# Kernel tuning notes

Hardware: AMD Instinct MI355X
Metric: run time of the kernel (lower is better)

## Reference

```python
import jax, jax.numpy as jnp
import numpy as np
from jax import lax

EPS_NORM = 1e-12   # F.normalize default eps
KS = 3             # fixed 3x3 window
K2 = KS * KS
MIN_CONN, MAX_CONN = 1, 8
NUM_GROUPS = 16    # largest divisor <=16 of C=128
GN_EPS = 1e-5


def _unfold3x3_reflect(x):
    # x: [B,C,H,W] -> patches [B,C,9,H,W] (reflect-padded 3x3 neighborhoods)
    B, C, H, W = x.shape
    p = jnp.pad(x, ((0, 0), (0, 0), (1, 1), (1, 1)), mode='reflect')
    pats = [p[:, :, dy:dy + H, dx:dx + W] for dy in range(KS) for dx in range(KS)]
    return jnp.stack(pats, axis=2)


def _df_counts(x):
    # DFDetector: mean over C, fixed Laplacian conv (zero pad), abs, per-batch min-max norm
    B = x.shape[0]
    avg = jnp.mean(x, axis=1, keepdims=True)  # [B,1,H,W]
    kern = jnp.array([[0., -1., 0.], [-1., 4., -1.], [0., -1., 0.]],
                     dtype=x.dtype).reshape(1, 1, 3, 3)
    df = jnp.abs(lax.conv_general_dilated(
        avg, kern, window_strides=(1, 1), padding=((1, 1), (1, 1)),
        dimension_numbers=('NCHW', 'OIHW', 'NCHW')))
    dmin = df.reshape(B, -1).min(axis=1).reshape(B, 1, 1, 1)
    dmax = df.reshape(B, -1).max(axis=1).reshape(B, 1, 1, 1)
    dn = (df - dmin) / (dmax - dmin + 1e-8)
    return MIN_CONN + jnp.round(dn * (MAX_CONN - MIN_CONN))  # [B,1,H,W], values in [1,8]


def _group_norm(x, w, b):
    B, C, H, W = x.shape
    g = x.reshape(B, NUM_GROUPS, -1)
    mu = g.mean(-1, keepdims=True)
    var = g.var(-1, keepdims=True)  # biased, matches torch GroupNorm
    g = (g - mu) * lax.rsqrt(var + GN_EPS)
    return g.reshape(B, C, H, W) * w[None, :, None, None] + b[None, :, None, None]


def setup_inputs() -> dict:
    key = jax.random.key(0)
    ks = jax.random.split(key, 7)
    B, C, H, W = 8, 128, 96, 96
    return {
        'x': jax.random.normal(ks[0], (B, C, H, W), jnp.float32),
        'gn_weight': jax.random.uniform(ks[1], (C,), jnp.float32, 0.5, 1.5),
        'gn_bias': jax.random.normal(ks[2], (C,), jnp.float32) * 0.1,
        'w1': jax.random.normal(ks[3], (2 * C, C), jnp.float32) * 0.02,
        'b1': jax.random.normal(ks[4], (2 * C,), jnp.float32) * 0.02,
        'w2': jax.random.normal(ks[5], (C, 2 * C), jnp.float32) * 0.02,
        'b2': jax.random.normal(ks[6], (C,), jnp.float32) * 0.02,
    }


def reference(x, gn_weight, gn_bias, w1, b1, w2, b2):
    B, C, H, W = x.shape
    P = H * W
    # per-pixel connection counts (integer k in [1,8]); non-differentiable in original
    counts = lax.stop_gradient(_df_counts(x))
    kvals = jnp.minimum(counts, K2).astype(jnp.int32).reshape(B, 1, P)

    patches = _unfold3x3_reflect(x).reshape(B, C, K2, P)
    xc = x.reshape(B, C, P)
    # L2 normalize over channel dim (F.normalize, eps=1e-12)
    cn = xc / jnp.maximum(jnp.linalg.norm(xc, axis=1, keepdims=True), EPS_NORM)
    pn = patches / jnp.maximum(jnp.linalg.norm(patches, axis=1, keepdims=True), EPS_NORM)

    sim = jnp.einsum('bcp,bckp->bkp', cn, pn)          # [B,9,P] cosine sims
    order = jnp.argsort(-sim, axis=1)                   # descending (== topk order)
    top_sim = jnp.take_along_axis(sim, order, axis=1)
    mask = jnp.arange(K2)[None, :, None] < kvals        # rank < k -> selected
    wts = jnp.exp(top_sim) * mask
    wts = wts / jnp.sum(wts, axis=1, keepdims=True)     # softmax over selected sims

    pat_sorted = jnp.take_along_axis(patches, order[:, None, :, :], axis=2)
    out = jnp.einsum('bckp,bkp->bcp', pat_sorted, wts).reshape(B, C, H, W)

    enhanced = out + _group_norm(x, gn_weight, gn_bias)
    h = jax.nn.relu(jnp.einsum('oi,bihw->bohw', w1, enhanced) + b1[None, :, None, None])
    ffn = jnp.einsum('oi,bihw->bohw', w2, h) + b2[None, :, None, None]
    return enhanced + ffn
```

## Files before the change

kernel.cpp:

```cpp
#include <hip/hip_runtime.h>

#define BD 8
#define CD 128
#define HD 96
#define WD 96
#define PD 9216
#define ND 73728

typedef __attribute__((ext_vector_type(8))) short short8;
typedef __attribute__((ext_vector_type(4))) float f32x4;

__device__ inline float bfu2f(unsigned int u) { return __uint_as_float(u << 16); }
__device__ inline unsigned short f2bfu(float f) {
  unsigned int u = __float_as_uint(f);
  u += 0x7fffu + ((u >> 16) & 1u);
  return (unsigned short)(u >> 16);
}

template<bool F32>
__device__ __forceinline__ float ldv(const void* __restrict__ p, size_t i) {
  if constexpr (F32) return ((const float*)p)[i];
  else return bfu2f(((const unsigned short*)p)[i]);
}

__global__ void k_detect(const unsigned int* __restrict__ xw, int* __restrict__ dcnt) {
  __shared__ int wl[4], we[4];
  const int t = threadIdx.x;
  uint4 w = ((const uint4*)xw)[blockIdx.x * 256 + t];
  int lz = (int)((w.x & 0xFFFFu) == 0u) + (int)((w.y & 0xFFFFu) == 0u) +
           (int)((w.z & 0xFFFFu) == 0u) + (int)((w.w & 0xFFFFu) == 0u);
  int e2 = (int)(((w.x >> 7) & 0xFFu) == 0xFFu) + (int)(((w.y >> 7) & 0xFFu) == 0xFFu) +
           (int)(((w.z >> 7) & 0xFFu) == 0xFFu) + (int)(((w.w >> 7) & 0xFFu) == 0xFFu);
  #pragma unroll
  for (int off = 32; off; off >>= 1) {
    lz += __shfl_down(lz, off);
    e2 += __shfl_down(e2, off);
  }
  if ((t & 63) == 0) { wl[t >> 6] = lz; we[t >> 6] = e2; }
  __syncthreads();
  if (t == 0) {
    dcnt[blockIdx.x] = wl[0] + wl[1] + wl[2] + wl[3];
    dcnt[64 + blockIdx.x] = we[0] + we[1] + we[2] + we[3];
  }
}

__global__ void k_cvt(const void* __restrict__ w1, const void* __restrict__ w2,
                      const void* __restrict__ gw, const void* __restrict__ gb,
                      const void* __restrict__ b1, const void* __restrict__ b2,
                      const int* __restrict__ dcnt,
                      unsigned short* __restrict__ wc, float* __restrict__ prm,
                      int* __restrict__ flag, unsigned long long* __restrict__ dmm) {
  __shared__ int sflag;
  const int t = threadIdx.x;
  if (t < 64) {
    int lz = dcnt[t], e2 = dcnt[64 + t];
    #pragma unroll
    for (int off = 32; off; off >>= 1) {
      lz += __shfl_down(lz, off);
      e2 += __shfl_down(e2, off);
    }
    if (t == 0) sflag = (lz > 4096 || e2 > 0) ? 1 : 0;
  }
  __syncthreads();
  const bool f32 = sflag != 0;
  const int blk = blockIdx.x;
  if (blk < 256) {
    int i = blk * 256 + t;
    if (i < 32768)
      wc[i] = f32 ? f2bfu(((const float*)w1)[i]) : ((const unsigned short*)w1)[i];
    else {
      int u = i - 32768;
      wc[i] = f32 ? f2bfu(((const float*)w2)[u]) : ((const unsigned short*)w2)[u];
    }
  } else {
    for (int i = t; i < 640; i += 256) {
      float v;
      if (i < 128)      v = f32 ? ((const float*)gw)[i]       : bfu2f(((const unsigned short*)gw)[i]);
      else if (i < 256) v = f32 ? ((const float*)gb)[i - 128] : bfu2f(((const unsigned short*)gb)[i - 128]);
      else if (i < 512) v = f32 ? ((const float*)b1)[i - 256] : bfu2f(((const unsigned short*)b1)[i - 256]);
      else              v = f32 ? ((const float*)b2)[i - 512] : bfu2f(((const unsigned short*)b2)[i - 512]);
      prm[i] = v;
    }
    if (t < 8) dmm[t] = 0x7FEFFFFFFFFFFFFFULL;
    else if (t < 16) dmm[t - 8 + 8] = 0ULL;
    if (t == 16) *flag = sflag;
  }
}

template<bool F32>
__device__ __forceinline__ void stats_body(const void* __restrict__ x,
                                           double* __restrict__ avg, double* __restrict__ nrm,
                                           double* __restrict__ nrm2, double* __restrict__ gpart,
                                           int lb) {
  const int t = threadIdx.x;
  const int gp0 = lb * 256;
  const int b = gp0 / PD, p0 = gp0 - b * PD;
  const size_t base = (size_t)b * CD * PD + p0 + t;
  double s = 0.0, q = 0.0;
  double qq0 = 0.0, qq1 = 0.0, qq2 = 0.0, qq3 = 0.0;
  double* gslot = gpart + (size_t)(lb * 4 + (t >> 6)) * 32;
  #pragma unroll
  for (int g = 0; g < 16; ++g) {
    double gs = 0.0, gq = 0.0;
    #pragma unroll
    for (int j = 0; j < 8; ++j) {
      const int c = g * 8 + j;
      double dv = (double)ldv<F32>(x, base + (size_t)c * PD);
      s += dv;
      q += dv * dv;
      if (g < 4) qq0 += dv * dv;
      else if (g < 8) qq1 += dv * dv;
      else if (g < 12) qq2 += dv * dv;
      else qq3 += dv * dv;
      gs += dv;
      gq += dv * dv;
    }
    #pragma unroll
    for (int off = 32; off; off >>= 1) {
      gs += __shfl_down(gs, off);
      gq += __shfl_down(gq, off);
    }
    if ((t & 63) == 0) { gslot[g * 2] = gs; gslot[g * 2 + 1] = gq; }
  }
  avg[gp0 + t] = s * (1.0 / 128.0);
  nrm[gp0 + t] = sqrt(q);
  nrm2[gp0 + t] = ((qq0 + qq1) + qq2) + qq3;
}
__global__ __launch_bounds__(256) void k_stats(const void* __restrict__ x,
                                               const int* __restrict__ flag,
                                               double* __restrict__ avg,
                                               double* __restrict__ nrm,
                                               double* __restrict__ nrm2,
                                               double* __restrict__ gpart) {
  const int lb = (blockIdx.x & 7) * 36 + (blockIdx.x >> 3);
  if (*flag) stats_body<true>(x, avg, nrm, nrm2, gpart, lb);
  else stats_body<false>(x, avg, nrm, nrm2, gpart, lb);
}

__device__ inline double lap_df(const double* __restrict__ a, int b, int y, int x) {
  const double* ab = a + (size_t)b * PD;
  double v = 4.0 * ab[y * WD + x];
  if (y > 0)      v -= ab[(y - 1) * WD + x];
  if (y < HD - 1) v -= ab[(y + 1) * WD + x];
  if (x > 0)      v -= ab[y * WD + x - 1];
  if (x < WD - 1) v -= ab[y * WD + x + 1];
  return fabs(v);
}

__global__ void k_mg(const double* __restrict__ avg, unsigned long long* __restrict__ dmm,
                     double* __restrict__ dfb, const double* __restrict__ gpart,
                     float* __restrict__ gn) {
  __shared__ double red[8];
  const int t = threadIdx.x;
  if (blockIdx.x < 288) {
    const int lb = ((int)blockIdx.x & 7) * 36 + ((int)blockIdx.x >> 3);
    int gp = lb * 256 + t;
    int b = gp / PD, p = gp - b * PD;
    double df = lap_df(avg, b, p / WD, p % WD);
    dfb[gp] = df;
    double mn = df, mx = df;
    #pragma unroll
    for (int off = 32; off; off >>= 1) {
      mn = fmin(mn, __shfl_down(mn, off));
      mx = fmax(mx, __shfl_down(mx, off));
    }
    if ((t & 63) == 0) { red[t >> 6] = mn; red[4 + (t >> 6)] = mx; }
    __syncthreads();
    if (t == 0) {
      mn = fmin(fmin(red[0], red[1]), fmin(red[2], red[3]));
      mx = fmax(fmax(red[4], red[5]), fmax(red[6], red[7]));
      atomicMin(&dmm[b], (unsigned long long)__double_as_longlong(mn));
      atomicMax(&dmm[b + 8], (unsigned long long)__double_as_longlong(mx));
    }
  } else {
    const int bg = blockIdx.x - 288;
    const int b = bg >> 4, g = bg & 15;
    double s = 0.0, q = 0.0;
    if (t < 144) {
      const double* pp = gpart + (size_t)(b * 144 + t) * 32 + g * 2;
      s = pp[0];
      q = pp[1];
    }
    #pragma unroll
    for (int off = 32; off; off >>= 1) {
      s += __shfl_down(s, off);
      q += __shfl_down(q, off);
    }
    if ((t & 63) == 0) { red[t >> 6] = s; red[4 + (t >> 6)] = q; }
    __syncthreads();
    if (t == 0) {
      double S = ((red[0] + red[1]) + red[2]) + red[3];
      double Q = ((red[4] + red[5]) + red[6]) + red[7];
      double mu = S / 73728.0;
      double var = Q / 73728.0 - mu * mu;
      gn[bg] = (float)mu;
      gn[128 + bg] = (float)(1.0 / sqrt(var + 1e-5));
    }
  }
}

template<bool F32>
__device__ __forceinline__ void ipg_body(const void* __restrict__ x,
                                         const double* __restrict__ nrm,
                                         const double* __restrict__ nrm2,
                                         const double* __restrict__ dfb,
                                         const unsigned long long* __restrict__ dmm,
                                         const float* __restrict__ gn,
                                         const float* __restrict__ prm,
                                         unsigned short* __restrict__ eg,
                                         float* __restrict__ tileF,
                                         double* __restrict__ nsl, double* __restrict__ nsl2) {
  float4* tile4 = (float4*)tileF;
  const float* gwf = prm;
  const float* gbf = prm + 128;

  const int t = threadIdx.x;
  const int lb = (blockIdx.x & 7) * 144 + (blockIdx.x >> 3);
  const int b = lb / 144;
  const int tid = lb - b * 144;
  const int ty = tid / 12, tx = tid - ty * 12;
  const int y0 = ty * 8, x0 = tx * 8;

  {
    const int hp = t & 127;
    if (hp < 100) {
      int hr = hp / 10, hc = hp - hr * 10;
      int gy = y0 - 1 + hr; gy = gy < 0 ? -gy : (gy >= HD ? 2 * HD - 2 - gy : gy);
      int gx = x0 - 1 + hc; gx = gx < 0 ? -gx : (gx >= WD ? 2 * WD - 2 - gx : gx);
      const size_t pbase = (size_t)b * CD * PD + (size_t)gy * WD + gx;
      const int sw = hp & 7;
      #pragma unroll
      for (int it = 0; it < 16; ++it) {
        int s = it * 2 + (t >> 7);
        size_t cb = pbase + (size_t)(4 * s) * PD;
        float4 v;
        v.x = ldv<F32>(x, cb);
        v.y = ldv<F32>(x, cb + PD);
        v.z = ldv<F32>(x, cb + 2 * PD);
        v.w = ldv<F32>(x, cb + 3 * PD);
        tile4[(hp * 32 + s) ^ sw] = v;
      }
      if (t < 100) nsl[t] = nrm[b * PD + gy * WD + gx];
    }
    if (t >= 128 && t < 192) {
      int a2 = t - 128;
      nsl2[a2] = nrm2[b * PD + (y0 + (a2 >> 3)) * WD + x0 + (a2 & 7)];
    }
  }
  __syncthreads();

  const int a = t >> 2, q = t & 3;
  const int yl = a >> 3, xl = a & 7;
  const int y = y0 + yl, xx = x0 + xl;
  const int p = y * WD + xx;
  const int cpix = (yl + 1) * 10 + (xl + 1);
  const int cub = cpix * 32 + q * 8, csw = cpix & 7;

  double sd[9];
  {
    float cv[32];
    #pragma unroll
    for (int j4 = 0; j4 < 8; ++j4)
      *(float4*)(cv + 4 * j4) = tile4[(cub + j4) ^ csw];
    #pragma unroll
    for (int k = 0; k < 9; ++k) {
      if (k == 4) continue;
      int dy = k / 3, dx = k - dy * 3;
      int pix = (yl + dy) * 10 + (xl + dx);
      int ub = pix * 32 + q * 8, sw = pix & 7;
      double acc = 0.0;
      #pragma unroll
      for (int seg = 0; seg < 8; ++seg) {
        float4 nv = tile4[(ub + seg) ^ sw];
        acc += (double)cv[seg * 4 + 0] * (double)nv.x;
        acc += (double)cv[seg * 4 + 1] * (double)nv.y;
        acc += (double)cv[seg * 4 + 2] * (double)nv.z;
        acc += (double)cv[seg * 4 + 3] * (double)nv.w;
      }
      double v1 = __shfl_down(acc, 1);
      double v2 = __shfl_down(acc, 2);
      double v3 = __shfl_down(acc, 3);
      sd[k] = ((acc + v1) + v2) + v3;
    }
  }

  float wv[9];
  #pragma unroll
  for (int j = 0; j < 9; ++j) wv[j] = 0.f;
  if (q == 0) {
    double dmin = __longlong_as_double((long long)dmm[b]);
    double dmax = __longlong_as_double((long long)dmm[b + 8]);
    double df = dfb[b * PD + p];
    double dn = (df - dmin) / (dmax - dmin + 1e-8);
    int kk = 1 + (int)rint(dn * 7.0);
    kk = kk < 1 ? 1 : (kk > 8 ? 8 : kk);

    sd[4] = nsl2[a];
    double np_ = fmax(nsl[cpix], 1e-12);
    #pragma unroll
    for (int k = 0; k < 9; ++k) {
      int dy = k / 3, dx = k - dy * 3;
      double nq = fmax(nsl[(yl + dy) * 10 + (xl + dx)], 1e-12);
      sd[k] = sd[k] / (np_ * nq);
    }
    float w[9];
    float wsum = 0.f;
    #pragma unroll
    for (int j = 0; j < 9; ++j) {
      int rank = 0;
      #pragma unroll
      for (int i = 0; i < 9; ++i)
        rank += (sd[i] > sd[j]) || (sd[i] == sd[j] && i < j);
      w[j] = (rank < kk) ? expf((float)sd[j]) : 0.f;
      wsum += w[j];
    }
    float inv = 1.f / wsum;
    #pragma unroll
    for (int j = 0; j < 9; ++j) wv[j] = w[j] * inv;
  }
  #pragma unroll
  for (int j = 0; j < 9; ++j) wv[j] = __shfl(wv[j], (t & 63) & ~3);

  {
    float og[32];
    #pragma unroll
    for (int j = 0; j < 32; ++j) og[j] = 0.f;
    #pragma unroll
    for (int k = 0; k < 9; ++k) {
      int dy = k / 3, dx = k - dy * 3;
      int pix = (yl + dy) * 10 + (xl + dx);
      int ub = pix * 32 + q * 8, sw = pix & 7;
      #pragma unroll
      for (int seg = 0; seg < 8; ++seg) {
        float4 nv = tile4[(ub + seg) ^ sw];
        og[seg * 4 + 0] += wv[k] * nv.x;
        og[seg * 4 + 1] += wv[k] * nv.y;
        og[seg * 4 + 2] += wv[k] * nv.z;
        og[seg * 4 + 3] += wv[k] * nv.w;
      }
    }
    const int g16 = b * 16;
    unsigned short* egr = eg + (size_t)(b * PD + p) * 128 + q * 32;
    #pragma unroll
    for (int seg = 0; seg < 4; ++seg) {
      float4 cA = tile4[(cub + seg * 2) ^ csw];
      float4 cB = tile4[(cub + seg * 2 + 1) ^ csw];
      float cvv[8] = {cA.x, cA.y, cA.z, cA.w, cB.x, cB.y, cB.z, cB.w};
      int g = q * 4 + seg;
      float mu = gn[g16 + g], rs = gn[128 + g16 + g];
      unsigned int pkd[4];
      #pragma unroll
      for (int j = 0; j < 8; ++j) {
        int c = q * 32 + seg * 8 + j;
        float e = og[seg * 8 + j] + (cvv[j] - mu) * rs * gwf[c] + gbf[c];
        unsigned int h = (unsigned int)f2bfu(e);
        if (j & 1) pkd[j >> 1] |= h << 16;
        else pkd[j >> 1] = h;
      }
      uint4 v; v.x = pkd[0]; v.y = pkd[1]; v.z = pkd[2]; v.w = pkd[3];
      *(uint4*)(egr + seg * 8) = v;
    }
  }
}
__global__ __launch_bounds__(256, 3) void k_ipg(const void* __restrict__ x,
                                                const int* __restrict__ flag,
                                                const double* __restrict__ nrm,
                                                const double* __restrict__ nrm2,
                                                const double* __restrict__ dfb,
                                                const unsigned long long* __restrict__ dmm,
                                                const float* __restrict__ gn,
                                                const float* __restrict__ prm,
                                                unsigned short* __restrict__ eg) {
  __shared__ float tileF[12800];
  __shared__ double nsl[100];
  __shared__ double nsl2[64];
  if (*flag) ipg_body<true>(x, nrm, nrm2, dfb, dmm, gn, prm, eg, tileF, nsl, nsl2);
  else ipg_body<false>(x, nrm, nrm2, dfb, dmm, gn, prm, eg, tileF, nsl, nsl2);
}

__global__ __launch_bounds__(256, 3) void k_ffn(const unsigned short* __restrict__ eg,
                                                const float* __restrict__ prm,
                                                const unsigned short* __restrict__ wc,
                                                float* __restrict__ outp) {
  __shared__ unsigned short et[64][136];
  __shared__ unsigned short Hl[64][264];
  const float* b1f = prm + 256;
  const float* b2f = prm + 512;

  const int t = threadIdx.x;
  const int lb = (blockIdx.x & 7) * 144 + (blockIdx.x >> 3);
  const int gp0 = lb * 64;
  const int b = gp0 / PD, p0b = gp0 - b * PD;

  const unsigned short* wc1 = wc;
  const unsigned short* wc2 = wc + 32768;
  const int lane = t & 63, wave = t >> 6;
  const int r16 = lane & 15, quad = lane >> 4;

  {
    const uint4* eg4 = (const uint4*)(eg + (size_t)gp0 * 128);
    #pragma unroll
    for (int it = 0; it < 4; ++it) {
      int lin = it * 256 + t;
      int row = lin >> 4, c8 = lin & 15;
      *(uint4*)&et[row][c8 * 8] = eg4[lin];
    }
  }
  short8 wb1[16];
  #pragma unroll
  for (int kk = 0; kk < 4; ++kk)
    #pragma unroll
    for (int nt = 0; nt < 4; ++nt)
      wb1[kk * 4 + nt] = *(const short8*)(wc1 + (size_t)(wave * 64 + nt * 16 + r16) * 128 + kk * 32 + quad * 8);
  __syncthreads();

  f32x4 acc[16];
  #pragma unroll
  for (int i = 0; i < 16; ++i) acc[i] = (f32x4){0.f, 0.f, 0.f, 0.f};
  #pragma unroll
  for (int kk = 0; kk < 4; ++kk) {
    short8 afm[4];
    #pragma unroll
    for (int m = 0; m < 4; ++m)
      afm[m] = *(const short8*)&et[m * 16 + r16][kk * 32 + quad * 8];
    #pragma unroll
    for (int nt = 0; nt < 4; ++nt)
      #pragma unroll
      for (int m = 0; m < 4; ++m)
        acc[m * 4 + nt] = __builtin_amdgcn_mfma_f32_16x16x32_bf16(afm[m], wb1[kk * 4 + nt], acc[m * 4 + nt], 0, 0, 0);
  }
  #pragma unroll
  for (int nt = 0; nt < 4; ++nt) {
    int n = wave * 64 + nt * 16 + r16;
    float bias = b1f[n];
    #pragma unroll
    for (int m = 0; m < 4; ++m)
      #pragma unroll
      for (int r = 0; r < 4; ++r)
        Hl[m * 16 + quad * 4 + r][n] = f2bfu(fmaxf(acc[m * 4 + nt][r] + bias, 0.f));
  }
  short8 wb2[16];
  #pragma unroll
  for (int kk = 0; kk < 8; ++kk)
    #pragma unroll
    for (int nt = 0; nt < 2; ++nt)
      wb2[kk * 2 + nt] = *(const short8*)(wc2 + (size_t)(wave * 32 + nt * 16 + r16) * 256 + kk * 32 + quad * 8);
  __syncthreads();

  f32x4 acc2[8];
  #pragma unroll
  for (int i = 0; i < 8; ++i) acc2[i] = (f32x4){0.f, 0.f, 0.f, 0.f};
  #pragma unroll
  for (int kk = 0; kk < 8; ++kk) {
    short8 afm[4];
    #pragma unroll
    for (int m = 0; m < 4; ++m)
      afm[m] = *(const short8*)&Hl[m * 16 + r16][kk * 32 + quad * 8];
    #pragma unroll
    for (int nt = 0; nt < 2; ++nt)
      #pragma unroll
      for (int m = 0; m < 4; ++m)
        acc2[m * 2 + nt] = __builtin_amdgcn_mfma_f32_16x16x32_bf16(afm[m], wb2[kk * 2 + nt], acc2[m * 2 + nt], 0, 0, 0);
  }
  #pragma unroll
  for (int nt = 0; nt < 2; ++nt) {
    int n = wave * 32 + nt * 16 + r16;
    float bias = b2f[n];
    #pragma unroll
    for (int m = 0; m < 4; ++m) {
      int mloc0 = m * 16 + quad * 4;
      float4 o;
      o.x = acc2[m * 2 + nt][0] + bias + bfu2f(et[mloc0 + 0][n]);
      o.y = acc2[m * 2 + nt][1] + bias + bfu2f(et[mloc0 + 1][n]);
      o.z = acc2[m * 2 + nt][2] + bias + bfu2f(et[mloc0 + 2][n]);
      o.w = acc2[m * 2 + nt][3] + bias + bfu2f(et[mloc0 + 3][n]);
      *(float4*)(outp + (size_t)(b * CD + n) * PD + p0b + mloc0) = o;
    }
  }
}

extern "C" void kernel_launch(void* const* d_in, const int* in_sizes, int n_in,
                              void* d_out, int out_size, void* d_ws, size_t ws_size,
                              hipStream_t stream) {
  const void* x  = d_in[0];
  const void* gw = d_in[1];
  const void* gb = d_in[2];
  const void* w1 = d_in[3];
  const void* b1 = d_in[4];
  const void* w2 = d_in[5];
  const void* b2 = d_in[6];
  float* out = (float*)d_out;

  char* ws = (char*)d_ws;
  int* flag = (int*)ws;
  int* dcnt = (int*)(ws + 16);
  unsigned long long* dmm = (unsigned long long*)(ws + 640);
  float* gn = (float*)(ws + 768);
  float* prm = (float*)(ws + 1792);
  unsigned short* wc = (unsigned short*)(ws + 4352);
  double* avg = (double*)(ws + 135424);
  double* nrm = (double*)(ws + 725248);
  double* nrm2 = (double*)(ws + 1315072);
  double* gpart = (double*)(ws + 1904896);
  double* dfb = (double*)(ws + 2199808);
  unsigned short* eg = (unsigned short*)(ws + 2789632);

  k_detect<<<64, 256, 0, stream>>>((const unsigned int*)x, dcnt);
  k_cvt<<<257, 256, 0, stream>>>(w1, w2, gw, gb, b1, b2, dcnt, wc, prm, flag, dmm);
  k_stats<<<288, 256, 0, stream>>>(x, flag, avg, nrm, nrm2, gpart);
  k_mg<<<416, 256, 0, stream>>>(avg, dmm, dfb, gpart, gn);
  k_ipg<<<ND / 64, 256, 0, stream>>>(x, flag, nrm, nrm2, dfb, dmm, gn, prm, eg);
  k_ffn<<<ND / 64, 256, 0, stream>>>(eg, prm, wc, out);
}
```

Before: 210.6 us.

## Transpose input to pixel-major layout in stats pass for coalesced halo loads

Replaces the stats kernel with one that loads 64-pixel by 128-channel tiles, computes the same statistics, and writes a pixel-major (channel-contiguous) copy of x to workspace. The patch kernel then gathers its 10x10 halo with contiguous float4 or ushort4 loads per pixel instead of strided per-channel scalar loads. This removes uncoalesced, channel-strided reads in k_ipg. In exchange it adds a full extra write and read of x through the workspace, and the bf16 path rounds the copy. The per-pixel stats now come from a single thread per pixel looping over shared memory.

```diff
diff --git a/kernel.cpp b/kernel.cpp
--- a/kernel.cpp
+++ b/kernel.cpp
@@ -82,59 +82,93 @@
       prm[i] = v;
     }
     if (t < 8) dmm[t] = 0x7FEFFFFFFFFFFFFFULL;
-    else if (t < 16) dmm[t - 8 + 8] = 0ULL;
+    else if (t < 16) dmm[t] = 0ULL;
     if (t == 16) *flag = sflag;
   }
 }
 
 template<bool F32>
-__device__ __forceinline__ void stats_body(const void* __restrict__ x,
-                                           double* __restrict__ avg, double* __restrict__ nrm,
-                                           double* __restrict__ nrm2, double* __restrict__ gpart,
-                                           int lb) {
-  const int t = threadIdx.x;
-  const int gp0 = lb * 256;
-  const int b = gp0 / PD, p0 = gp0 - b * PD;
-  const size_t base = (size_t)b * CD * PD + p0 + t;
-  double s = 0.0, q = 0.0;
-  double qq0 = 0.0, qq1 = 0.0, qq2 = 0.0, qq3 = 0.0;
-  double* gslot = gpart + (size_t)(lb * 4 + (t >> 6)) * 32;
-  #pragma unroll
-  for (int g = 0; g < 16; ++g) {
-    double gs = 0.0, gq = 0.0;
-    #pragma unroll
-    for (int j = 0; j < 8; ++j) {
-      const int c = g * 8 + j;
-      double dv = (double)ldv<F32>(x, base + (size_t)c * PD);
-      s += dv;
-      q += dv * dv;
-      if (g < 4) qq0 += dv * dv;
-      else if (g < 8) qq1 += dv * dv;
-      else if (g < 12) qq2 += dv * dv;
-      else qq3 += dv * dv;
-      gs += dv;
-      gq += dv * dv;
-    }
+__device__ __forceinline__ void pmt_body(const void* __restrict__ x,
+                                         void* __restrict__ xpm,
+                                         double* __restrict__ avg, double* __restrict__ nrm,
+                                         double* __restrict__ nrm2,
+                                         double* __restrict__ gpart,
+                                         float (*tile)[132], int lb) {
+  const int t = threadIdx.x, px = t & 63, ci = t >> 6;
+  const int gp0 = lb * 64, b = gp0 / PD, p0 = gp0 - b * PD;
+  double sg[4] = {0.0, 0.0, 0.0, 0.0}, qg[4] = {0.0, 0.0, 0.0, 0.0};
+  for (int j = 0; j < 32; ++j) {
+    int c = ci * 32 + j;
+    float v = ldv<F32>(x, (size_t)(b * CD + c) * PD + p0 + px);
+    tile[px][c] = v;
+    sg[j >> 3] += (double)v;
+    qg[j >> 3] += (double)v * (double)v;
+  }
+  #pragma unroll
+  for (int g = 0; g < 4; ++g) {
     #pragma unroll
     for (int off = 32; off; off >>= 1) {
-      gs += __shfl_down(gs, off);
-      gq += __shfl_down(gq, off);
-    }
-    if ((t & 63) == 0) { gslot[g * 2] = gs; gslot[g * 2 + 1] = gq; }
-  }
-  avg[gp0 + t] = s * (1.0 / 128.0);
-  nrm[gp0 + t] = sqrt(q);
-  nrm2[gp0 + t] = ((qq0 + qq1) + qq2) + qq3;
-}
-__global__ __launch_bounds__(256) void k_stats(const void* __restrict__ x,
-                                               const int* __restrict__ flag,
-                                               double* __restrict__ avg,
-                                               double* __restrict__ nrm,
-                                               double* __restrict__ nrm2,
-                                               double* __restrict__ gpart) {
-  const int lb = (blockIdx.x & 7) * 36 + (blockIdx.x >> 3);
-  if (*flag) stats_body<true>(x, avg, nrm, nrm2, gpart, lb);
-  else stats_body<false>(x, avg, nrm, nrm2, gpart, lb);
+      sg[g] += __shfl_down(sg[g], off);
+      qg[g] += __shfl_down(qg[g], off);
+    }
+  }
+  if (px == 0) {
+    double* gp_ = gpart + (size_t)lb * 32;
+    #pragma unroll
+    for (int g = 0; g < 4; ++g) {
+      gp_[(ci * 4 + g) * 2 + 0] = sg[g];
+      gp_[(ci * 4 + g) * 2 + 1] = qg[g];
+    }
+  }
+  __syncthreads();
+  if constexpr (F32) {
+    float* xo = (float*)xpm;
+    for (int i = t; i < 2048; i += 256) {
+      int r = i >> 5, seg = i & 31;
+      *(float4*)(xo + (size_t)(gp0 + r) * 128 + seg * 4) = *(const float4*)&tile[r][seg * 4];
+    }
+  } else {
+    unsigned short* xo = (unsigned short*)xpm;
+    for (int i = t; i < 2048; i += 256) {
+      int r = i >> 5, seg = i & 31;
+      ushort4 v;
+      v.x = f2bfu(tile[r][seg * 4 + 0]);
+      v.y = f2bfu(tile[r][seg * 4 + 1]);
+      v.z = f2bfu(tile[r][seg * 4 + 2]);
+      v.w = f2bfu(tile[r][seg * 4 + 3]);
+      *(ushort4*)(xo + (size_t)(gp0 + r) * 128 + seg * 4) = v;
+    }
+  }
+  if (t < 64) {
+    double s = 0.0, q = 0.0;
+    for (int c = 0; c < 128; ++c) {
+      float v = tile[t][c];
+      s += (double)v;
+      q += (double)v * (double)v;
+    }
+    double qq[4] = {0.0, 0.0, 0.0, 0.0};
+    #pragma unroll
+    for (int g = 0; g < 4; ++g)
+      for (int i = 0; i < 32; ++i) {
+        float v = tile[t][g * 32 + i];
+        qq[g] += (double)v * (double)v;
+      }
+    avg[gp0 + t] = s * (1.0 / 128.0);
+    nrm[gp0 + t] = sqrt(q);
+    nrm2[gp0 + t] = ((qq[0] + qq[1]) + qq[2]) + qq[3];
+  }
+}
+__global__ __launch_bounds__(256) void k_pmt(const void* __restrict__ x,
+                                             const int* __restrict__ flag,
+                                             void* __restrict__ xpm,
+                                             double* __restrict__ avg,
+                                             double* __restrict__ nrm,
+                                             double* __restrict__ nrm2,
+                                             double* __restrict__ gpart) {
+  __shared__ float tile[64][132];
+  const int lb = (blockIdx.x & 7) * 144 + (blockIdx.x >> 3);
+  if (*flag) pmt_body<true>(x, xpm, avg, nrm, nrm2, gpart, tile, lb);
+  else pmt_body<false>(x, xpm, avg, nrm, nrm2, gpart, tile, lb);
 }
 
 __device__ inline double lap_df(const double* __restrict__ a, int b, int y, int x) {
@@ -200,7 +234,7 @@
 }
 
 template<bool F32>
-__device__ __forceinline__ void ipg_body(const void* __restrict__ x,
+__device__ __forceinline__ void ipg_body(const void* __restrict__ xpm,
                                          const double* __restrict__ nrm,
                                          const double* __restrict__ nrm2,
                                          const double* __restrict__ dfb,
@@ -222,27 +256,30 @@
   const int y0 = ty * 8, x0 = tx * 8;
 
   {
-    const int hp = t & 127;
-    if (hp < 100) {
-      int hr = hp / 10, hc = hp - hr * 10;
+    const int s = t & 31, hpb = t >> 5;
+    #pragma unroll
+    for (int it = 0; it < 13; ++it) {
+      int hp = it * 8 + hpb;
+      if (hp < 100) {
+        int hr = hp / 10, hc = hp - hr * 10;
+        int gy = y0 - 1 + hr; gy = gy < 0 ? -gy : (gy >= HD ? 2 * HD - 2 - gy : gy);
+        int gx = x0 - 1 + hc; gx = gx < 0 ? -gx : (gx >= WD ? 2 * WD - 2 - gx : gx);
+        float4 v;
+        if constexpr (F32) {
+          v = *((const float4*)((const float*)xpm + (size_t)(b * PD + gy * WD + gx) * 128) + s);
+        } else {
+          ushort4 u = *((const ushort4*)((const unsigned short*)xpm + (size_t)(b * PD + gy * WD + gx) * 128) + s);
+          v.x = bfu2f(u.x); v.y = bfu2f(u.y); v.z = bfu2f(u.z); v.w = bfu2f(u.w);
+        }
+        tile4[(hp * 32 + s) ^ (hp & 7)] = v;
+      }
+    }
+    if (t < 100) {
+      int hr = t / 10, hc = t - hr * 10;
       int gy = y0 - 1 + hr; gy = gy < 0 ? -gy : (gy >= HD ? 2 * HD - 2 - gy : gy);
       int gx = x0 - 1 + hc; gx = gx < 0 ? -gx : (gx >= WD ? 2 * WD - 2 - gx : gx);
-      const size_t pbase = (size_t)b * CD * PD + (size_t)gy * WD + gx;
-      const int sw = hp & 7;
-      #pragma unroll
-      for (int it = 0; it < 16; ++it) {
-        int s = it * 2 + (t >> 7);
-        size_t cb = pbase + (size_t)(4 * s) * PD;
-        float4 v;
-        v.x = ldv<F32>(x, cb);
-        v.y = ldv<F32>(x, cb + PD);
-        v.z = ldv<F32>(x, cb + 2 * PD);
-        v.w = ldv<F32>(x, cb + 3 * PD);
-        tile4[(hp * 32 + s) ^ sw] = v;
-      }
-      if (t < 100) nsl[t] = nrm[b * PD + gy * WD + gx];
-    }
-    if (t >= 128 && t < 192) {
+      nsl[t] = nrm[b * PD + gy * WD + gx];
+    } else if (t >= 128 && t < 192) {
       int a2 = t - 128;
       nsl2[a2] = nrm2[b * PD + (y0 + (a2 >> 3)) * WD + x0 + (a2 & 7)];
     }
@@ -362,7 +399,7 @@
     }
   }
 }
-__global__ __launch_bounds__(256, 3) void k_ipg(const void* __restrict__ x,
+__global__ __launch_bounds__(256, 3) void k_ipg(const void* __restrict__ xpm,
                                                 const int* __restrict__ flag,
                                                 const double* __restrict__ nrm,
                                                 const double* __restrict__ nrm2,
@@ -374,8 +411,8 @@
   __shared__ float tileF[12800];
   __shared__ double nsl[100];
   __shared__ double nsl2[64];
-  if (*flag) ipg_body<true>(x, nrm, nrm2, dfb, dmm, gn, prm, eg, tileF, nsl, nsl2);
-  else ipg_body<false>(x, nrm, nrm2, dfb, dmm, gn, prm, eg, tileF, nsl, nsl2);
+  if (*flag) ipg_body<true>(xpm, nrm, nrm2, dfb, dmm, gn, prm, eg, tileF, nsl, nsl2);
+  else ipg_body<false>(xpm, nrm, nrm2, dfb, dmm, gn, prm, eg, tileF, nsl, nsl2);
 }
 
 __global__ __launch_bounds__(256, 3) void k_ffn(const unsigned short* __restrict__ eg,
@@ -504,11 +541,12 @@
   double* gpart = (double*)(ws + 1904896);
   double* dfb = (double*)(ws + 2199808);
   unsigned short* eg = (unsigned short*)(ws + 2789632);
+  void* xpm = (void*)(ws + 21664000);
 
   k_detect<<<64, 256, 0, stream>>>((const unsigned int*)x, dcnt);
   k_cvt<<<257, 256, 0, stream>>>(w1, w2, gw, gb, b1, b2, dcnt, wc, prm, flag, dmm);
-  k_stats<<<288, 256, 0, stream>>>(x, flag, avg, nrm, nrm2, gpart);
+  k_pmt<<<ND / 64, 256, 0, stream>>>(x, flag, xpm, avg, nrm, nrm2, gpart);
   k_mg<<<416, 256, 0, stream>>>(avg, dmm, dfb, gpart, gn);
-  k_ipg<<<ND / 64, 256, 0, stream>>>(x, flag, nrm, nrm2, dfb, dmm, gn, prm, eg);
+  k_ipg<<<ND / 64, 256, 0, stream>>>(xpm, flag, nrm, nrm2, dfb, dmm, gn, prm, eg);
   k_ffn<<<ND / 64, 256, 0, stream>>>(eg, prm, wc, out);
 }
```

Result: faster. 194.2 us (-7.8%).
